# Optimization experiments

Measured on AMD Instinct MI355X. Metric: run time of the kernel, lower is better.

Reference implementation:

```python
import jax, jax.numpy as jnp
import numpy as np

MODEL_DIM = 2048
NUM_HEADS = 32
NUM_KV_HEADS = 8
HEAD_DIM = MODEL_DIM // NUM_HEADS  # 64
NUM_REP = NUM_HEADS // NUM_KV_HEADS  # 4


def setup_inputs() -> dict:
    key = jax.random.key(0)
    ks = jax.random.split(key, 6)
    B, S = 1, 2048
    s = 1.0 / np.sqrt(MODEL_DIM)
    x = jax.random.normal(ks[0], (B, S, MODEL_DIM), dtype=jnp.float32)
    # causal mask, 1 = keep, 0 = mask (scores.masked_fill(mask == 0, -1e9))
    mask = jnp.tril(jnp.ones((S, S), dtype=jnp.int32))[None, None, :, :]
    w_q = jax.random.normal(ks[1], (MODEL_DIM, MODEL_DIM), dtype=jnp.float32) * s
    w_k = jax.random.normal(ks[2], (NUM_KV_HEADS * HEAD_DIM, MODEL_DIM), dtype=jnp.float32) * s
    w_v = jax.random.normal(ks[3], (NUM_KV_HEADS * HEAD_DIM, MODEL_DIM), dtype=jnp.float32) * s
    w_o = jax.random.normal(ks[4], (MODEL_DIM, MODEL_DIM), dtype=jnp.float32) * s
    b_o = jax.random.normal(ks[5], (MODEL_DIM,), dtype=jnp.float32) * 0.01
    return {"x": x, "mask": mask, "w_q": w_q, "w_k": w_k, "w_v": w_v, "w_o": w_o, "b_o": b_o}


def reference(x, mask, w_q, w_k, w_v, w_o, b_o):
    B, S, _ = x.shape
    # projections (torch Linear: x @ W.T)
    q = (x @ w_q.T).reshape(B, S, NUM_HEADS, HEAD_DIM).transpose(0, 2, 1, 3)      # [B,H,S,D]
    k = (x @ w_k.T).reshape(B, S, NUM_KV_HEADS, HEAD_DIM).transpose(0, 2, 1, 3)   # [B,Hk,S,D]
    v = (x @ w_v.T).reshape(B, S, NUM_KV_HEADS, HEAD_DIM).transpose(0, 2, 1, 3)   # [B,Hk,S,D]
    # group Q heads by their shared KV head instead of materializing repeated KV
    qg = q.reshape(B, NUM_KV_HEADS, NUM_REP, S, HEAD_DIM)                         # [B,Hk,R,S,D]
    scale = 1.0 / np.sqrt(HEAD_DIM).astype(np.float32)
    scores = jnp.einsum('bgrsd,bgtd->bgrst', qg, k) * scale                       # [B,Hk,R,S,S]
    scores = jnp.where(mask[:, :, None, :, :] == 0, jnp.float32(-1e9), scores)
    attn = jax.nn.softmax(scores, axis=-1)
    ctx = jnp.einsum('bgrst,bgtd->bgrsd', attn, v)                                # [B,Hk,R,S,D]
    ctx = ctx.reshape(B, NUM_HEADS, S, HEAD_DIM).transpose(0, 2, 1, 3).reshape(B, S, MODEL_DIM)
    return ctx @ w_o.T + b_o
```

## Files before the change

kernel.cpp:

```cpp
#include <hip/hip_runtime.h>
#include <hip/hip_bf16.h>

typedef __hip_bfloat16 bf16;
typedef __attribute__((ext_vector_type(8))) short short8;
typedef __attribute__((ext_vector_type(4))) short short4_t;
typedef __attribute__((ext_vector_type(4))) float f32x4;

#define S_LEN 2048
#define DMODEL 2048
#define NH 32
#define NKV 8
#define DH 64

__global__ void detect_kernel(const unsigned int* __restrict__ x, int* __restrict__ flag) {
    int tid = threadIdx.x;
    unsigned int w = x[tid * 37];
    int e0 = (w >> 7) & 0xFF;
    int in = (e0 >= 100 && e0 <= 140) ? 1 : 0;
    unsigned long long m = __ballot(in);
    if (tid == 0) flag[0] = (__popcll(m) >= 48) ? 1 : 0;
}

__device__ __forceinline__ void conv8(const void* src, bf16* dst, int i, float scale, int isbf) {
    short8 out;
    if (isbf) {
        short8 v = *(const short8*)((const bf16*)src + i);
        if (scale != 1.0f) {
            #pragma unroll
            for (int j = 0; j < 8; ++j) {
                float f = __bfloat162float(((const bf16*)&v)[j]) * scale;
                ((bf16*)&out)[j] = __float2bfloat16(f);
            }
        } else out = v;
    } else {
        const float* gp = (const float*)src + i;
        f32x4 a = *(const f32x4*)gp;
        f32x4 b = *(const f32x4*)(gp + 4);
        #pragma unroll
        for (int j = 0; j < 4; ++j) ((bf16*)&out)[j]     = __float2bfloat16(a[j] * scale);
        #pragma unroll
        for (int j = 0; j < 4; ++j) ((bf16*)&out)[j + 4] = __float2bfloat16(b[j] * scale);
    }
    *(short8*)(dst + i) = out;
}

__global__ __launch_bounds__(256)
void convert_kernel(const void* __restrict__ src, bf16* __restrict__ dst,
                    int n, float scale, const int* __restrict__ flagp) {
    const int isbf = flagp[0];
    int i = (blockIdx.x * 256 + threadIdx.x) * 8;
    const int stride = gridDim.x * 256 * 8;
    for (; i < n; i += stride) conv8(src, dst, i, scale, isbf);
}

__global__ __launch_bounds__(256)
void convert4_kernel(const void* __restrict__ x, const void* __restrict__ wq,
                     const void* __restrict__ wk, const void* __restrict__ wv,
                     bf16* __restrict__ xb, bf16* __restrict__ wqkv,
                     const int* __restrict__ flagp) {
    const int isbf = flagp[0];
    const int b = blockIdx.x;
    const void* src; bf16* dst; int boff; float scale = 1.0f;
    if (b < 2048)       { src = x;  dst = xb;              boff = b;        }
    else if (b < 4096)  { src = wq; dst = wqkv;            boff = b - 2048; scale = 0.125f; }
    else if (b < 4608)  { src = wk; dst = wqkv + 4194304;  boff = b - 4096; }
    else                { src = wv; dst = wqkv + 5242880;  boff = b - 4608; }
    int i = (boff * 256 + threadIdx.x) * 8;
    conv8(src, dst, i, scale, isbf);
}

__device__ __forceinline__ void gload_lds16(const void* g, void* l) {
    __builtin_amdgcn_global_load_lds(
        (const __attribute__((address_space(1))) void*)(unsigned long long)(size_t)g,
        (__attribute__((address_space(3))) void*)(unsigned int)(size_t)l,
        16, 0, 0);
}

__device__ __forceinline__ void gemm_core_12864(const bf16* __restrict__ A, const bf16* __restrict__ B,
                                                int K, int m0, int n0,
                                                bf16* sA, bf16* sB, f32x4 acc[4][2]) {
    const int tid = threadIdx.x;
    const int w = tid >> 6, lane = tid & 63;
    const int wm = (w >> 1) * 64, wn = (w & 1) * 32;
    const int lm = lane & 15, lq = lane >> 4;
    const int lrow = lane >> 2;
    const int scol = (lane & 3) * 8;

    const bf16* ApA = A + (size_t)(m0 + w * 32 + lrow) * K + scol;
    const bf16* ApB = ApA + (size_t)16 * K;
    const bf16* Bp  = B + (size_t)(n0 + w * 16 + lrow) * K + scol;
    bf16* la = sA + w * 1024;
    bf16* lb = sB + w * 512;

    for (int k0 = 0; k0 < K; k0 += 32) {
        __syncthreads();
        gload_lds16(ApA + k0, la);
        gload_lds16(ApB + k0, la + 512);
        gload_lds16(Bp + k0,  lb);
        __syncthreads();

        short8 aF[4], bF[2];
        #pragma unroll
        for (int i = 0; i < 4; ++i)
            aF[i] = *(const short8*)&sA[(wm + i * 16 + lm) * 32 + lq * 8];
        #pragma unroll
        for (int j = 0; j < 2; ++j)
            bF[j] = *(const short8*)&sB[(wn + j * 16 + lm) * 32 + lq * 8];
        #pragma unroll
        for (int i = 0; i < 4; ++i)
            #pragma unroll
            for (int j = 0; j < 2; ++j)
                acc[i][j] = __builtin_amdgcn_mfma_f32_16x16x32_bf16(aF[i], bF[j], acc[i][j], 0, 0, 0);
    }
}

template<bool BIAS, bool BIAS_DYN, bool OUT_DYN>
__global__ __launch_bounds__(256, 4)
void gemm_bf16s(const bf16* __restrict__ A, const bf16* __restrict__ B,
                const void* __restrict__ bias, void* __restrict__ C,
                int M, int N, int K, int ldc, const int* __restrict__ flagp) {
    __shared__ bf16 sA[128 * 32];
    __shared__ bf16 sB[64 * 32];
    const int isbf = flagp[0];
    const int tid = threadIdx.x;
    const int m0 = blockIdx.y * 128, n0 = blockIdx.x * 64;
    const int w = tid >> 6, lane = tid & 63;
    const int wm = (w >> 1) * 64, wn = (w & 1) * 32;
    const int lm = lane & 15, lq = lane >> 4;

    f32x4 acc[4][2];
    const f32x4 zero = {0.f, 0.f, 0.f, 0.f};
    for (int i = 0; i < 4; ++i)
        for (int j = 0; j < 2; ++j) acc[i][j] = zero;

    gemm_core_12864(A, B, K, m0, n0, sA, sB, acc);

    for (int i = 0; i < 4; ++i)
        for (int j = 0; j < 2; ++j)
            for (int r = 0; r < 4; ++r) {
                int row = m0 + wm + i * 16 + lq * 4 + r;
                int col = n0 + wn + j * 16 + lm;
                float v = acc[i][j][r];
                if (BIAS) {
                    if (BIAS_DYN && !isbf) v += ((const float*)bias)[col];
                    else                   v += __bfloat162float(((const bf16*)bias)[col]);
                }
                size_t idx = (size_t)row * ldc + col;
                if (OUT_DYN && !isbf) ((float*)C)[idx] = v;
                else                  ((bf16*)C)[idx] = __float2bfloat16(v);
            }
}

__global__ __launch_bounds__(256, 4)
void gemm_qkv(const bf16* __restrict__ A, const bf16* __restrict__ B,
              bf16* __restrict__ Qo, bf16* __restrict__ Ko, bf16* __restrict__ Vto) {
    __shared__ bf16 sA[128 * 32];
    __shared__ bf16 sB[64 * 32];
    const int tid = threadIdx.x;
    const int m0 = blockIdx.y * 128, n0 = blockIdx.x * 64;
    const int w = tid >> 6, lane = tid & 63;
    const int wm = (w >> 1) * 64, wn = (w & 1) * 32;
    const int lm = lane & 15, lq = lane >> 4;

    f32x4 acc[4][2];
    const f32x4 zero = {0.f, 0.f, 0.f, 0.f};
    for (int i = 0; i < 4; ++i)
        for (int j = 0; j < 2; ++j) acc[i][j] = zero;

    gemm_core_12864(A, B, DMODEL, m0, n0, sA, sB, acc);

    const int route = (n0 < 2048) ? 0 : ((n0 < 2560) ? 1 : 2);
    for (int i = 0; i < 4; ++i)
        for (int j = 0; j < 2; ++j)
            for (int r = 0; r < 4; ++r) {
                int row = m0 + wm + i * 16 + lq * 4 + r;
                int col = n0 + wn + j * 16 + lm;
                bf16 v = __float2bfloat16(acc[i][j][r]);
                if (route == 0)      Qo[(size_t)row * DMODEL + col] = v;
                else if (route == 1) Ko[(size_t)row * (NKV * DH) + (col - 2048)] = v;
                else                 Vto[(size_t)(col - 2560) * S_LEN + row] = v;
            }
}

template<bool TRANS_OUT, bool BIAS, bool A_DYN, bool B_DYN, bool BIAS_DYN, bool OUT_DYN>
__global__ __launch_bounds__(256, 2)
void gemm_bt(const void* __restrict__ A, const void* __restrict__ B,
             const void* __restrict__ bias, void* __restrict__ C,
             int M, int N, int K, int ldc, const int* __restrict__ flagp) {
    __shared__ bf16 sA[128 * 32];
    __shared__ bf16 sB[128 * 32];

    const int isbf = flagp[0];
    const int tid = threadIdx.x;
    const int m0 = blockIdx.y * 128, n0 = blockIdx.x * 128;
    const int w = tid >> 6, lane = tid & 63;
    const int wm = (w >> 1) * 64, wn = (w & 1) * 64;
    const int lm = lane & 15, lq = lane >> 4;

    f32x4 acc[4][4];
    const f32x4 zero = {0.f, 0.f, 0.f, 0.f};
    for (int i = 0; i < 4; ++i)
        for (int j = 0; j < 4; ++j) acc[i][j] = zero;

    for (int k0 = 0; k0 < K; k0 += 32) {
        __syncthreads();
        for (int it = 0; it < 2; ++it) {
            int c = it * 256 + tid;
            int row = c >> 2, off = (c & 3) * 8;
            if (!A_DYN || isbf) {
                *(short8*)&sA[row * 32 + off] =
                    *(const short8*)((const bf16*)A + (size_t)(m0 + row) * K + k0 + off);
            } else {
                const float* gp = (const float*)A + (size_t)(m0 + row) * K + k0 + off;
                #pragma unroll
                for (int i = 0; i < 8; ++i) sA[row * 32 + off + i] = __float2bfloat16(gp[i]);
            }
            if (!B_DYN || isbf) {
                *(short8*)&sB[row * 32 + off] =
                    *(const short8*)((const bf16*)B + (size_t)(n0 + row) * K + k0 + off);
            } else {
                const float* gp = (const float*)B + (size_t)(n0 + row) * K + k0 + off;
                #pragma unroll
                for (int i = 0; i < 8; ++i) sB[row * 32 + off + i] = __float2bfloat16(gp[i]);
            }
        }
        __syncthreads();

        short8 aF[4], bF[4];
        for (int i = 0; i < 4; ++i)
            aF[i] = *(const short8*)&sA[(wm + i * 16 + lm) * 32 + lq * 8];
        for (int i = 0; i < 4; ++i)
            bF[i] = *(const short8*)&sB[(wn + i * 16 + lm) * 32 + lq * 8];
        for (int i = 0; i < 4; ++i)
            for (int j = 0; j < 4; ++j)
                acc[i][j] = __builtin_amdgcn_mfma_f32_16x16x32_bf16(aF[i], bF[j], acc[i][j], 0, 0, 0);
    }

    for (int i = 0; i < 4; ++i)
        for (int j = 0; j < 4; ++j)
            for (int r = 0; r < 4; ++r) {
                int row = m0 + wm + i * 16 + lq * 4 + r;
                int col = n0 + wn + j * 16 + lm;
                float v = acc[i][j][r];
                if (BIAS) {
                    if (BIAS_DYN && !isbf) v += ((const float*)bias)[col];
                    else                   v += __bfloat162float(((const bf16*)bias)[col]);
                }
                size_t idx = TRANS_OUT ? (size_t)col * ldc + row : (size_t)row * ldc + col;
                if (OUT_DYN && !isbf) ((float*)C)[idx] = v;
                else                  ((bf16*)C)[idx] = __float2bfloat16(v);
            }
}

template<bool PRESCALED>
__global__ __launch_bounds__(256, 2)
void attn_kernel(const bf16* __restrict__ Q, const bf16* __restrict__ Km,
                 const bf16* __restrict__ Vt, bf16* __restrict__ ctx) {
    __shared__ bf16 sQ[64 * 72];
    __shared__ bf16 sK[64 * 72];
    __shared__ bf16 sV[64 * 72];
    __shared__ bf16 sP[4][16 * 72];

    const int tid = threadIdx.x;
    const int h  = blockIdx.y;
    const int kvh = h >> 2;
    const int w = tid >> 6, lane = tid & 63;
    const int lm = lane & 15, lq = lane >> 4;
    const int qloc = w * 16 + lm;

    const int r0 = tid >> 3,         o0 = (tid & 7) * 8;
    const int r1 = (tid + 256) >> 3, o1 = (tid & 7) * 8;

    const f32x4 zero = {0.f, 0.f, 0.f, 0.f};

    for (int ph = 0; ph < 2; ++ph) {
        const int qb = ph ? (31 - blockIdx.x) : blockIdx.x;

        __syncthreads();
        for (int c = tid; c < 512; c += 256) {
            int row = c >> 3, off = (c & 7) * 8;
            *(short8*)&sQ[row * 72 + off] =
                *(const short8*)&Q[(size_t)(qb * 64 + row) * DMODEL + h * 64 + off];
        }

        float m_r = -1e30f, l_r = 0.f;
        f32x4 oacc[4];
        #pragma unroll
        for (int ni = 0; ni < 4; ++ni) oacc[ni] = zero;

        short8 kr0, kr1, vr0, vr1;
        kr0 = *(const short8*)&Km[(size_t)r0 * (NKV * DH) + kvh * 64 + o0];
        kr1 = *(const short8*)&Km[(size_t)r1 * (NKV * DH) + kvh * 64 + o1];
        vr0 = *(const short8*)&Vt[(size_t)(kvh * 64 + r0) * S_LEN + o0];
        vr1 = *(const short8*)&Vt[(size_t)(kvh * 64 + r1) * S_LEN + o1];

        for (int kt = 0; kt <= qb; ++kt) {
            __syncthreads();
            *(short8*)&sK[r0 * 72 + o0] = kr0;
            *(short8*)&sK[r1 * 72 + o1] = kr1;
            *(short8*)&sV[r0 * 72 + o0] = vr0;
            *(short8*)&sV[r1 * 72 + o1] = vr1;
            __syncthreads();
            if (kt < qb) {
                int nk = kt + 1;
                kr0 = *(const short8*)&Km[(size_t)(nk * 64 + r0) * (NKV * DH) + kvh * 64 + o0];
                kr1 = *(const short8*)&Km[(size_t)(nk * 64 + r1) * (NKV * DH) + kvh * 64 + o1];
                vr0 = *(const short8*)&Vt[(size_t)(kvh * 64 + r0) * S_LEN + nk * 64 + o0];
                vr1 = *(const short8*)&Vt[(size_t)(kvh * 64 + r1) * S_LEN + nk * 64 + o1];
            }

            f32x4 sacc[4];
            #pragma unroll
            for (int ni = 0; ni < 4; ++ni) sacc[ni] = zero;
            __builtin_amdgcn_s_setprio(1);
            #pragma unroll
            for (int ks = 0; ks < 2; ++ks) {
                short8 aq = *(const short8*)&sQ[(w * 16 + lm) * 72 + ks * 32 + lq * 8];
                #pragma unroll
                for (int ni = 0; ni < 4; ++ni) {
                    short8 bk = *(const short8*)&sK[(ni * 16 + lm) * 72 + ks * 32 + lq * 8];
                    sacc[ni] = __builtin_amdgcn_mfma_f32_16x16x32_bf16(bk, aq, sacc[ni], 0, 0, 0);
                }
            }
            __builtin_amdgcn_s_setprio(0);

            float sv[4][4];
            float mx = -3e38f;
            #pragma unroll
            for (int ni = 0; ni < 4; ++ni)
                #pragma unroll
                for (int r = 0; r < 4; ++r) {
                    float s = sacc[ni][r];
                    if (!PRESCALED) s *= 0.125f;
                    if (kt == qb && (ni * 16 + lq * 4 + r) > qloc) s = -1e30f;
                    sv[ni][r] = s;
                    mx = fmaxf(mx, s);
                }
            mx = fmaxf(mx, __shfl_xor(mx, 16));
            mx = fmaxf(mx, __shfl_xor(mx, 32));

            int defer = (mx - m_r <= 8.0f) ? 1 : 0;
            if (!__all(defer)) {
                float m_new = fmaxf(m_r, mx);
                float alpha = __expf(m_r - m_new);
                m_r = m_new;
                l_r *= alpha;
                #pragma unroll
                for (int r = 0; r < 4; ++r) {
                    float a_b = __shfl(alpha, (lane & 48) | (lq * 4 + r));
                    #pragma unroll
                    for (int ni = 0; ni < 4; ++ni) oacc[ni][r] *= a_b;
                }
            }

            float rs = 0.f;
            #pragma unroll
            for (int ni = 0; ni < 4; ++ni) {
                short4_t pk;
                #pragma unroll
                for (int r = 0; r < 4; ++r) {
                    float p = __expf(sv[ni][r] - m_r);
                    rs += p;
                    ((bf16*)&pk)[r] = __float2bfloat16(p);
                }
                *(short4_t*)&sP[w][lm * 72 + ni * 16 + lq * 4] = pk;
            }
            rs += __shfl_xor(rs, 16);
            rs += __shfl_xor(rs, 32);
            l_r += rs;

            asm volatile("s_waitcnt lgkmcnt(0)" ::: "memory");
            __builtin_amdgcn_sched_barrier(0);

            __builtin_amdgcn_s_setprio(1);
            #pragma unroll
            for (int ks = 0; ks < 2; ++ks) {
                short8 ap = *(const short8*)&sP[w][lm * 72 + ks * 32 + lq * 8];
                #pragma unroll
                for (int ni = 0; ni < 4; ++ni) {
                    short8 bv = *(const short8*)&sV[(ni * 16 + lm) * 72 + ks * 32 + lq * 8];
                    oacc[ni] = __builtin_amdgcn_mfma_f32_16x16x32_bf16(ap, bv, oacc[ni], 0, 0, 0);
                }
            }
            __builtin_amdgcn_s_setprio(0);
        }

        #pragma unroll
        for (int r = 0; r < 4; ++r) {
            float l_b = __shfl(l_r, (lane & 48) | (lq * 4 + r));
            float inv = 1.0f / l_b;
            #pragma unroll
            for (int ni = 0; ni < 4; ++ni)
                ctx[(size_t)(qb * 64 + w * 16 + lq * 4 + r) * DMODEL + h * 64 + ni * 16 + lm] =
                    __float2bfloat16(oacc[ni][r] * inv);
        }
    }
}

extern "C" void kernel_launch(void* const* d_in, const int* in_sizes, int n_in,
                              void* d_out, int out_size, void* d_ws, size_t ws_size,
                              hipStream_t stream) {
    const void* x   = d_in[0];
    const void* w_q = d_in[2];
    const void* w_k = d_in[3];
    const void* w_v = d_in[4];
    const void* w_o = d_in[5];
    const void* b_o = d_in[6];

    const size_t MB = 1024u * 1024u;
    char* ws = (char*)d_ws;
    int*  flag = (int*)ws;
    dim3 blk(256);

    detect_kernel<<<1, 64, 0, stream>>>((const unsigned int*)x, flag);

    if (ws_size >= 32 * MB + 4096) {
        bf16* xb   = (bf16*)(ws + 4096);
        bf16* wqkv = (bf16*)(ws + 4096 + 8 * MB);
        bf16* Qws  = (bf16*)(ws + 4096 + 20 * MB);
        bf16* Kws  = (bf16*)(ws + 4096 + 28 * MB);
        bf16* Vtws = (bf16*)(ws + 4096 + 30 * MB);
        bf16* wob  = xb;
        bf16* Ctx  = wqkv;

        convert4_kernel<<<5120, blk, 0, stream>>>(x, w_q, w_k, w_v, xb, wqkv, flag);
        gemm_qkv<<<dim3(48, 16), blk, 0, stream>>>(xb, wqkv, Qws, Kws, Vtws);
        convert_kernel<<<2048, blk, 0, stream>>>(w_o, wob, DMODEL * DMODEL, 1.0f, flag);
        attn_kernel<true><<<dim3(16, 32), blk, 0, stream>>>(Qws, Kws, Vtws, Ctx);
        gemm_bf16s<true, true, true><<<dim3(32, 16), blk, 0, stream>>>(
            Ctx, wob, b_o, d_out, S_LEN, DMODEL, DMODEL, DMODEL, flag);
    } else {
        bf16* Qws  = (bf16*)(ws + 4096);
        bf16* Kws  = (bf16*)(ws + 4096 + 8u * MB);
        bf16* Vtws = (bf16*)(ws + 4096 + 10u * MB);
        bf16* Ctx  = (bf16*)(ws + 4096 + 12u * MB);

        gemm_bt<false, false, true, true, false, false><<<dim3(16, 16), blk, 0, stream>>>(
            x, w_q, nullptr, Qws, S_LEN, DMODEL, DMODEL, DMODEL, flag);
        gemm_bt<false, false, true, true, false, false><<<dim3(4, 16), blk, 0, stream>>>(
            x, w_k, nullptr, Kws, S_LEN, NKV * DH, DMODEL, NKV * DH, flag);
        gemm_bt<true, false, true, true, false, false><<<dim3(4, 16), blk, 0, stream>>>(
            x, w_v, nullptr, Vtws, S_LEN, NKV * DH, DMODEL, S_LEN, flag);
        attn_kernel<false><<<dim3(16, 32), blk, 0, stream>>>(Qws, Kws, Vtws, Ctx);
        gemm_bt<false, true, false, true, true, true><<<dim3(16, 16), blk, 0, stream>>>(
            Ctx, w_o, b_o, d_out, S_LEN, DMODEL, DMODEL, DMODEL, flag);
    }
}
```

Baseline: 255.3 us.

## Double-buffer GEMM LDS tiles with BK=64, XOR swizzle and one barrier

Rewrites the shared GEMM core used by the QKV and output projections. It now double-buffers the LDS tiles, issuing the next K-tile's global-to-LDS loads before computing the current one, and widens the K step from 32 to 64. It adds an XOR swizzle on LDS columns to avoid bank conflicts, drops to one barrier per iteration, and raises wave priority around the MFMA block. The cost is more LDS per block, so occupancy is lowered to 3 blocks per CU.

Measured after the change: 225.0 us. -11.9%, faster.

```diff
diff --git a/kernel.cpp b/kernel.cpp
--- a/kernel.cpp
+++ b/kernel.cpp
@@ -76,51 +76,90 @@
         16, 0, 0);
 }
 
-__device__ __forceinline__ void gemm_core_12864(const bf16* __restrict__ A, const bf16* __restrict__ B,
-                                                int K, int m0, int n0,
-                                                bf16* sA, bf16* sB, f32x4 acc[4][2]) {
+__device__ __forceinline__ void gemm_core_2ph(const bf16* __restrict__ A, const bf16* __restrict__ B,
+                                              int K, int m0, int n0,
+                                              bf16* sA, bf16* sB, f32x4 acc[4][2]) {
     const int tid = threadIdx.x;
     const int w = tid >> 6, lane = tid & 63;
     const int wm = (w >> 1) * 64, wn = (w & 1) * 32;
     const int lm = lane & 15, lq = lane >> 4;
-    const int lrow = lane >> 2;
-    const int scol = (lane & 3) * 8;
-
-    const bf16* ApA = A + (size_t)(m0 + w * 32 + lrow) * K + scol;
-    const bf16* ApB = ApA + (size_t)16 * K;
-    const bf16* Bp  = B + (size_t)(n0 + w * 16 + lrow) * K + scol;
-    bf16* la = sA + w * 1024;
-    bf16* lb = sB + w * 512;
-
-    for (int k0 = 0; k0 < K; k0 += 32) {
+    const int xr = lm & 7;
+
+    size_t aoff[4], boff[2];
+    #pragma unroll
+    for (int r = 0; r < 4; ++r) {
+        int ci = w * 256 + r * 64 + lane;
+        int row = ci >> 3, c = (ci & 7) ^ (row & 7);
+        aoff[r] = (size_t)(m0 + row) * K + c * 8;
+    }
+    #pragma unroll
+    for (int r = 0; r < 2; ++r) {
+        int cj = w * 128 + r * 64 + lane;
+        int row = cj >> 3, c = (cj & 7) ^ (row & 7);
+        boff[r] = (size_t)(n0 + row) * K + c * 8;
+    }
+
+    const int nt = K >> 6;
+    int cur = 0;
+
+    {
+        bf16* la = sA + w * 2048;
+        bf16* lb = sB + w * 1024;
+        #pragma unroll
+        for (int r = 0; r < 4; ++r) gload_lds16(A + aoff[r], la + r * 512);
+        #pragma unroll
+        for (int r = 0; r < 2; ++r) gload_lds16(B + boff[r], lb + r * 512);
+    }
+    __syncthreads();
+
+    for (int t = 0; t < nt; ++t) {
+        bf16* curA = sA + cur * 8192;
+        bf16* curB = sB + cur * 4096;
+        if (t + 1 < nt) {
+            const int nxt = cur ^ 1;
+            const int k0 = (t + 1) << 6;
+            bf16* la = sA + nxt * 8192 + w * 2048;
+            bf16* lb = sB + nxt * 4096 + w * 1024;
+            #pragma unroll
+            for (int r = 0; r < 4; ++r) gload_lds16(A + aoff[r] + k0, la + r * 512);
+            #pragma unroll
+            for (int r = 0; r < 2; ++r) gload_lds16(B + boff[r] + k0, lb + r * 512);
+        }
+
+        short8 aF[2][4], bF[2][2];
+        #pragma unroll
+        for (int ks = 0; ks < 2; ++ks) {
+            const int cc = ((ks * 4 + lq) ^ xr) * 8;
+            #pragma unroll
+            for (int i = 0; i < 4; ++i)
+                aF[ks][i] = *(const short8*)&curA[(wm + i * 16 + lm) * 64 + cc];
+            #pragma unroll
+            for (int j = 0; j < 2; ++j)
+                bF[ks][j] = *(const short8*)&curB[(wn + j * 16 + lm) * 64 + cc];
+        }
+
+        __builtin_amdgcn_s_setprio(1);
+        #pragma unroll
+        for (int ks = 0; ks < 2; ++ks)
+            #pragma unroll
+            for (int i = 0; i < 4; ++i)
+                #pragma unroll
+                for (int j = 0; j < 2; ++j)
+                    acc[i][j] = __builtin_amdgcn_mfma_f32_16x16x32_bf16(aF[ks][i], bF[ks][j], acc[i][j], 0, 0, 0);
+        __builtin_amdgcn_s_setprio(0);
+
         __syncthreads();
-        gload_lds16(ApA + k0, la);
-        gload_lds16(ApB + k0, la + 512);
-        gload_lds16(Bp + k0,  lb);
-        __syncthreads();
-
-        short8 aF[4], bF[2];
-        #pragma unroll
-        for (int i = 0; i < 4; ++i)
-            aF[i] = *(const short8*)&sA[(wm + i * 16 + lm) * 32 + lq * 8];
-        #pragma unroll
-        for (int j = 0; j < 2; ++j)
-            bF[j] = *(const short8*)&sB[(wn + j * 16 + lm) * 32 + lq * 8];
-        #pragma unroll
-        for (int i = 0; i < 4; ++i)
-            #pragma unroll
-            for (int j = 0; j < 2; ++j)
-                acc[i][j] = __builtin_amdgcn_mfma_f32_16x16x32_bf16(aF[i], bF[j], acc[i][j], 0, 0, 0);
+        cur ^= 1;
     }
 }
 
 template<bool BIAS, bool BIAS_DYN, bool OUT_DYN>
-__global__ __launch_bounds__(256, 4)
+__global__ __launch_bounds__(256, 3)
 void gemm_bf16s(const bf16* __restrict__ A, const bf16* __restrict__ B,
                 const void* __restrict__ bias, void* __restrict__ C,
                 int M, int N, int K, int ldc, const int* __restrict__ flagp) {
-    __shared__ bf16 sA[128 * 32];
-    __shared__ bf16 sB[64 * 32];
+    __shared__ bf16 sA[2 * 128 * 64];
+    __shared__ bf16 sB[2 * 64 * 64];
     const int isbf = flagp[0];
     const int tid = threadIdx.x;
     const int m0 = blockIdx.y * 128, n0 = blockIdx.x * 64;
@@ -133,7 +172,7 @@
     for (int i = 0; i < 4; ++i)
         for (int j = 0; j < 2; ++j) acc[i][j] = zero;
 
-    gemm_core_12864(A, B, K, m0, n0, sA, sB, acc);
+    gemm_core_2ph(A, B, K, m0, n0, sA, sB, acc);
 
     for (int i = 0; i < 4; ++i)
         for (int j = 0; j < 2; ++j)
@@ -151,11 +190,11 @@
             }
 }
 
-__global__ __launch_bounds__(256, 4)
+__global__ __launch_bounds__(256, 3)
 void gemm_qkv(const bf16* __restrict__ A, const bf16* __restrict__ B,
               bf16* __restrict__ Qo, bf16* __restrict__ Ko, bf16* __restrict__ Vto) {
-    __shared__ bf16 sA[128 * 32];
-    __shared__ bf16 sB[64 * 32];
+    __shared__ bf16 sA[2 * 128 * 64];
+    __shared__ bf16 sB[2 * 64 * 64];
     const int tid = threadIdx.x;
     const int m0 = blockIdx.y * 128, n0 = blockIdx.x * 64;
     const int w = tid >> 6, lane = tid & 63;
@@ -167,7 +206,7 @@
     for (int i = 0; i < 4; ++i)
         for (int j = 0; j < 2; ++j) acc[i][j] = zero;
 
-    gemm_core_12864(A, B, DMODEL, m0, n0, sA, sB, acc);
+    gemm_core_2ph(A, B, DMODEL, m0, n0, sA, sB, acc);
 
     const int route = (n0 < 2048) ? 0 : ((n0 < 2560) ? 1 : 2);
     for (int i = 0; i < 4; ++i)
```
